# Kernel tuning notes

Measured on AMD Instinct MI355X. Metric: run time of the kernel, lower is better.

## Reference

```python
import jax, jax.numpy as jnp
import numpy as np
import math

EPS = 1e-6


def setup_inputs() -> dict:
    key = jax.random.key(0)
    k1, k2, k3 = jax.random.split(key, 3)
    B, S, D = 8, 2048, 256
    return {
        "query": jax.random.normal(k1, (B, S, D), dtype=jnp.float32),
        "keys": jax.random.normal(k2, (B, S, D), dtype=jnp.float32),
        "values": jax.random.normal(k3, (B, S, D), dtype=jnp.float32),
        "c": jnp.asarray(0.01, dtype=jnp.float32),  # learned curvature parameter
    }


def reference(query, keys, values, c):
    # query/keys: [B,S,D], values: [B,S,Dv]
    scale = math.sqrt(query.shape[-1])
    q2 = jnp.sum(query * query, axis=-1)            # [B,S]  |q_i|^2
    k2 = jnp.sum(keys * keys, axis=-1)              # [B,S]  |k_j|^2
    cross = jnp.einsum("bid,bjd->bij", query, keys)  # [B,S,S]
    # squared pairwise distance via identity, avoiding the [B,S,S,D] diff tensor
    nd2 = jnp.maximum(q2[:, :, None] + k2[:, None, :] - 2.0 * cross, 0.0)
    # faithful to original: denom pairs query row i with key row i (broadcast quirk)
    denom = jnp.maximum((1.0 - c * q2) * (1.0 - c * k2), EPS)  # [B,S]
    arg = jnp.maximum(1.0 + 2.0 * c * nd2 / denom[:, :, None], 1.0 + EPS)
    dist = jnp.arccosh(arg)                          # [B,S,S]
    attn = jax.nn.softmax(-dist / scale, axis=-1)
    return jnp.einsum("bij,bjd->bid", attn, values)
```

## Files before the change

kernel.cpp:

```cpp
#include <hip/hip_runtime.h>

#define B_N   8
#define S_LEN 2048
#define D_DIM 256

typedef __attribute__((ext_vector_type(4)))  float          f32x4;
typedef __attribute__((ext_vector_type(16))) float          f32x16;
typedef __attribute__((ext_vector_type(8)))  short          s16x8;
typedef __attribute__((ext_vector_type(8)))  __bf16         b16x8;
typedef __attribute__((ext_vector_type(8)))  unsigned short u16x8;
typedef __attribute__((ext_vector_type(4)))  unsigned int   u32x4;

__device__ __forceinline__ unsigned short f2bf(float f) {
    unsigned u = __builtin_bit_cast(unsigned, f);
    u += 0x7FFFu + ((u >> 16) & 1u);
    return (unsigned short)(u >> 16);
}
__device__ __forceinline__ u16x8 pack8(f32x4 a, f32x4 b) {
    u16x8 o;
#pragma unroll
    for (int u = 0; u < 4; ++u) { o[u] = f2bf(a[u]); o[u + 4] = f2bf(b[u]); }
    return o;
}
__device__ __forceinline__ f32x16 zero16() {
    f32x16 z;
#pragma unroll
    for (int i = 0; i < 16; ++i) z[i] = 0.f;
    return z;
}
__device__ __forceinline__ unsigned cvtpk(float lo, float hi) {
    unsigned r;
    asm("v_cvt_pk_bf16_f32 %0, %1, %2" : "=v"(r) : "v"(lo), "v"(hi));
    return r;
}
__device__ __forceinline__ void xswap(unsigned& x, unsigned& y, int lh) {
    unsigned vs = lh ? x : y;
    unsigned vr = (unsigned)__shfl_xor((int)vs, 32, 64);
    x = lh ? vr : x;
    y = lh ? y : vr;
}
__device__ __forceinline__ float hw_sqrt(float x) {
    float r; asm("v_sqrt_f32 %0, %1" : "=v"(r) : "v"(x)); return r;
}
__device__ __forceinline__ float hw_log2(float x) {
    float r; asm("v_log_f32 %0, %1" : "=v"(r) : "v"(x)); return r;
}
__device__ __forceinline__ float hw_exp2(float x) {
    float r; asm("v_exp_f32 %0, %1" : "=v"(r) : "v"(x)); return r;
}
__device__ __forceinline__ float hw_rcp(float x) {
    float r; asm("v_rcp_f32 %0, %1" : "=v"(r) : "v"(x)); return r;
}
__device__ __forceinline__ void gload16(const void* g, void* l) {
    __builtin_amdgcn_global_load_lds((const __attribute__((address_space(1))) void*)g,
                                     (__attribute__((address_space(3))) void*)l, 16, 0, 0);
}

template <typename A>
__device__ __forceinline__ auto mfma3216_(A a, A b, f32x16 c, int)
    -> decltype(__builtin_amdgcn_mfma_f32_32x32x16_bf16(a, b, c, 0, 0, 0)) {
    return __builtin_amdgcn_mfma_f32_32x32x16_bf16(a, b, c, 0, 0, 0);
}
template <typename A>
__device__ __forceinline__ f32x16 mfma3216_(A a, A b, f32x16 c, long) {
    b16x8 a2 = __builtin_bit_cast(b16x8, a);
    b16x8 b2 = __builtin_bit_cast(b16x8, b);
    return __builtin_amdgcn_mfma_f32_32x32x16_bf16(a2, b2, c, 0, 0, 0);
}
__device__ __forceinline__ f32x16 MFMA(u16x8 a, u16x8 b, f32x16 c) {
    return mfma3216_(__builtin_bit_cast(s16x8, a), __builtin_bit_cast(s16x8, b), c, 0);
}

__global__ void __launch_bounds__(256) prep_rows(const float* __restrict__ Q,
                                                 const float* __restrict__ K,
                                                 const float* __restrict__ cp,
                                                 float* __restrict__ q2g,
                                                 float* __restrict__ k2g,
                                                 float* __restrict__ cfg) {
    const int w = threadIdx.x >> 6, l = threadIdx.x & 63;
    const float c = *cp;
#pragma unroll 1
    for (int p = 0; p < 16; ++p) {
        const int row = blockIdx.x * 64 + p * 4 + w;
        f32x4 qv = *((const f32x4*)(Q + (size_t)row * D_DIM) + l);
        f32x4 kv = *((const f32x4*)(K + (size_t)row * D_DIM) + l);
        float sq = qv[0]*qv[0] + qv[1]*qv[1] + qv[2]*qv[2] + qv[3]*qv[3];
        float sk = kv[0]*kv[0] + kv[1]*kv[1] + kv[2]*kv[2] + kv[3]*kv[3];
#pragma unroll
        for (int m = 1; m < 64; m <<= 1) {
            sq += __shfl_xor(sq, m, 64);
            sk += __shfl_xor(sk, m, 64);
        }
        if (l == 0) {
            q2g[row] = sq;
            k2g[row] = sk;
            float dn = fmaxf((1.f - c * sq) * (1.f - c * sk), 1e-6f);
            cfg[row] = 2.f * c / dn;
        }
    }
}

__global__ void __launch_bounds__(256) cvt_bf16(const float* __restrict__ src,
                                                unsigned short* __restrict__ dst) {
    const size_t i = ((size_t)blockIdx.x * 256 + threadIdx.x) * 8;
    f32x4 a = *(const f32x4*)(src + i);
    f32x4 b = *(const f32x4*)(src + i + 4);
    *(u16x8*)(dst + i) = pack8(a, b);
}

__global__ void __launch_bounds__(256) transp_v(const float* __restrict__ V,
                                                unsigned short* __restrict__ VT) {
    __shared__ float tile[64][65];
    const int bid = blockIdx.x;
    const int b = bid >> 7, rem = bid & 127, jt = rem >> 2, dt = rem & 3;
    const int j0 = jt * 64, d0 = dt * 64;
    const int t = threadIdx.x;
#pragma unroll
    for (int p = 0; p < 4; ++p) {
        const int jr = p * 16 + (t >> 4);
        f32x4 v = *(const f32x4*)(V + (size_t)(b * S_LEN + j0 + jr) * D_DIM + d0 + (t & 15) * 4);
#pragma unroll
        for (int u = 0; u < 4; ++u) tile[jr][(t & 15) * 4 + u] = v[u];
    }
    __syncthreads();
#pragma unroll
    for (int p = 0; p < 2; ++p) {
        const int dr = p * 32 + (t >> 3), seg = t & 7;
        u16x8 o;
#pragma unroll
        for (int u = 0; u < 8; ++u) o[u] = f2bf(tile[seg * 8 + u][dr]);
        *(u16x8*)(VT + (size_t)(b * D_DIM + d0 + dr) * S_LEN + j0 + seg * 8) = o;
    }
}

template <int PRE>
__global__ void __launch_bounds__(256, 2) hyp_attn(
    const float* __restrict__ Qf, const float* __restrict__ Kf, const float* __restrict__ Vf,
    const unsigned short* __restrict__ Kb, const unsigned short* __restrict__ VTg,
    const float* __restrict__ q2g, const float* __restrict__ k2g, const float* __restrict__ cfg,
    float* __restrict__ out) {
    __shared__ __align__(1024) unsigned char tiles[65536];
    __shared__ float k2sh[S_LEN];
    __shared__ float lsumBuf[2][2][32];
    const int bid = blockIdx.x;
    const int nb = (bid & 7) * 64 + (bid >> 3);
    const int b = nb >> 6, rt = nb & 63;
    const int tid = threadIdx.x;
    const int w = tid >> 6, l = tid & 63;
    const int l31 = l & 31, lh = l >> 5;
    const int jsub = w & 1, dh = w >> 1;
    const int qr0 = rt * 32;
    const int qrow = b * S_LEN + qr0 + l31;

    *(f32x4*)&k2sh[tid * 8]     = *(const f32x4*)(k2g + b * S_LEN + tid * 8);
    *(f32x4*)&k2sh[tid * 8 + 4] = *(const f32x4*)(k2g + b * S_LEN + tid * 8 + 4);

    u16x8 qf[16];
    {
        const float* qp = Qf + (size_t)qrow * D_DIM + lh * 8;
#pragma unroll
        for (int ks = 0; ks < 16; ++ks) {
            f32x4 a = *(const f32x4*)(qp + ks * 16);
            f32x4 c4 = *(const f32x4*)(qp + ks * 16 + 4);
            qf[ks] = pack8(a, c4);
        }
    }
    const float q2r = q2g[qrow];
    const float cfr = cfg[qrow];
    const float base1 = fmaf(cfr, q2r, 1.0f);

    f32x16 oacc[4];
#pragma unroll
    for (int i = 0; i < 4; ++i) oacc[i] = zero16();
    float lsum = 0.f;

    const size_t kbBase = (size_t)b * S_LEN * D_DIM;

    auto stageK = [&](int buf, int it) {
        const int j0 = it * 64;
#pragma unroll
        for (int p = 0; p < 8; ++p) {
            const int idx = p * 256 + tid;
            const int row = idx >> 5, sl = idx & 31;
            const unsigned short* gp = Kb + kbBase + (size_t)(j0 + row) * D_DIM
                                     + ((sl ^ (row & 7)) << 3);
            gload16(gp, (char*)tiles + buf * 32768 + idx * 16);
        }
    };
    auto stageK0 = [&](int buf, int it) {
        const int j0 = it * 64;
#pragma unroll
        for (int p = 0; p < 8; ++p) {
            const int idx = p * 256 + tid;
            const int row = idx >> 5, sl = idx & 31;
            const float* sp = Kf + kbBase + (size_t)(j0 + row) * D_DIM
                            + ((sl ^ (row & 7)) << 3);
            *(u16x8*)((char*)tiles + buf * 32768 + idx * 16) =
                pack8(*(const f32x4*)sp, *(const f32x4*)(sp + 4));
        }
    };
    const unsigned short* vbase = VTg + ((size_t)(b * D_DIM + dh * 128 + l31) * S_LEN)
                                + jsub * 32 + lh * 8;
    auto loadVg = [&](int it, u16x8 (&Vr)[8]) {
        const unsigned short* p0 = vbase + it * 64;
#pragma unroll
        for (int db = 0; db < 4; ++db) {
            Vr[db * 2]     = *(const u16x8*)(p0 + (size_t)(db * 32) * S_LEN);
            Vr[db * 2 + 1] = *(const u16x8*)(p0 + (size_t)(db * 32) * S_LEN + 16);
        }
    };
    auto loadV0 = [&](int it, u16x8 (&Vr)[8]) {
        const int j0 = it * 64 + jsub * 32 + lh * 8;
#pragma unroll
        for (int db = 0; db < 4; ++db) {
            const int d = dh * 128 + db * 32 + l31;
            u16x8 o0, o1;
#pragma unroll
            for (int u = 0; u < 8; ++u) {
                o0[u] = f2bf(Vf[kbBase + (size_t)(j0 + u) * D_DIM + d]);
                o1[u] = f2bf(Vf[kbBase + (size_t)(j0 + 16 + u) * D_DIM + d]);
            }
            Vr[db * 2] = o0; Vr[db * 2 + 1] = o1;
        }
    };

    const int xk = (l31 & 7) << 4;
    const char* KBp = (const char*)tiles + (jsub * 32 + l31) * 512;

    auto qktF = [&](int buf) {
        f32x16 s = zero16();
#pragma unroll
        for (int ks = 0; ks < 16; ++ks) {
            u16x8 kf = *(const u16x8*)(KBp + buf * 32768 + (((ks * 2 + lh) << 4) ^ xk));
            s = MFMA(kf, qf[ks], s);
        }
        return s;
    };
    auto softmaxF = [&](int it, f32x16& s, u16x8& pa0, u16x8& pa1) {
        f32x4 k2q[4];
#pragma unroll
        for (int g = 0; g < 4; ++g)
            k2q[g] = *(const f32x4*)&k2sh[it * 64 + jsub * 32 + g * 8 + lh * 4];
#pragma unroll
        for (int r = 0; r < 16; ++r) {
            const float t = fmaf(-2.f, s[r], k2q[r >> 2][r & 3]);
            const float arg = fmaxf(fmaf(cfr, t, base1), 1.f + 1e-6f);
            const float y = arg + hw_sqrt(fmaf(arg, arg, -1.f));
            const float p = hw_exp2(hw_log2(y) * -0.0625f);
            lsum += p;
            s[r] = p;
        }
        unsigned A_ = cvtpk(s[0], s[1]),   C_ = cvtpk(s[2], s[3]);
        unsigned Bv = cvtpk(s[4], s[5]),   D_ = cvtpk(s[6], s[7]);
        unsigned E_ = cvtpk(s[8], s[9]),   G_ = cvtpk(s[10], s[11]);
        unsigned F_ = cvtpk(s[12], s[13]), H_ = cvtpk(s[14], s[15]);
        xswap(A_, Bv, lh); xswap(C_, D_, lh);
        xswap(E_, F_, lh); xswap(G_, H_, lh);
        pa0 = __builtin_bit_cast(u16x8, (u32x4){A_, C_, Bv, D_});
        pa1 = __builtin_bit_cast(u16x8, (u32x4){E_, G_, F_, H_});
    };
    auto pvF = [&](u16x8 pa0, u16x8 pa1, u16x8 (&VA)[8]) {
#pragma unroll
        for (int db = 0; db < 4; ++db) {
            oacc[db] = MFMA(pa0, VA[db * 2], oacc[db]);
            oacc[db] = MFMA(pa1, VA[db * 2 + 1], oacc[db]);
        }
    };

    if (PRE) {
        stageK(0, 0);
        asm volatile("s_waitcnt vmcnt(0) lgkmcnt(0)" ::: "memory");
        __builtin_amdgcn_s_barrier();
        f32x16 sacc = qktF(0);
#pragma unroll 1
        for (int it = 0; it < 32; ++it) {
            u16x8 VA[8];
            loadVg(it, VA);
            if (it < 31) stageK((it + 1) & 1, it + 1);
            u16x8 pa0, pa1;
            softmaxF(it, sacc, pa0, pa1);
            asm volatile("s_waitcnt vmcnt(0)" ::: "memory");
            __builtin_amdgcn_s_barrier();
            __builtin_amdgcn_s_setprio(1);
            pvF(pa0, pa1, VA);
            if (it < 31) sacc = qktF((it + 1) & 1);
            __builtin_amdgcn_s_setprio(0);
        }
    } else {
#pragma unroll 1
        for (int it = 0; it < 32; ++it) {
            u16x8 VA[8];
            stageK0(0, it);
            loadV0(it, VA);
            __syncthreads();
            f32x16 sacc = qktF(0);
            u16x8 pa0, pa1;
            softmaxF(it, sacc, pa0, pa1);
            pvF(pa0, pa1, VA);
            __syncthreads();
        }
    }

    lsum += __shfl_xor(lsum, 32, 64);
    if (lh == 0) lsumBuf[jsub][dh][l31] = lsum;
    float* sf = (float*)tiles;
    if (jsub == 1) {
#pragma unroll
        for (int db = 0; db < 4; ++db)
#pragma unroll
            for (int r = 0; r < 16; ++r) {
                const int crow = (r & 3) + 8 * (r >> 2) + 4 * lh;
                sf[dh * 4096 + crow * 128 + db * 32 + l31] = oacc[db][r];
            }
    }
    __syncthreads();
    if (jsub == 0) {
        float rdn[16];
#pragma unroll
        for (int r = 0; r < 16; ++r) {
            const int crow = (r & 3) + 8 * (r >> 2) + 4 * lh;
            rdn[r] = hw_rcp(lsumBuf[0][dh][crow] + lsumBuf[1][dh][crow]);
        }
#pragma unroll
        for (int db = 0; db < 4; ++db)
#pragma unroll
            for (int r = 0; r < 16; ++r) {
                const int crow = (r & 3) + 8 * (r >> 2) + 4 * lh;
                const float o = oacc[db][r] + sf[dh * 4096 + crow * 128 + db * 32 + l31];
                out[(size_t)(b * S_LEN + qr0 + crow) * D_DIM + dh * 128 + db * 32 + l31]
                    = o * rdn[r];
            }
    }
}

extern "C" void kernel_launch(void* const* d_in, const int* in_sizes, int n_in,
                              void* d_out, int out_size, void* d_ws, size_t ws_size,
                              hipStream_t stream) {
    const float* Q = (const float*)d_in[0];
    const float* K = (const float*)d_in[1];
    const float* V = (const float*)d_in[2];
    const float* cp = (const float*)d_in[3];
    float* out = (float*)d_out;
    (void)in_sizes; (void)n_in; (void)out_size;

    const size_t BS = (size_t)B_N * S_LEN;
    float* q2g = (float*)d_ws;
    float* k2g = q2g + BS;
    float* cfg = k2g + BS;
    unsigned short* Kb = (unsigned short*)(cfg + BS);
    unsigned short* VTg = Kb + BS * D_DIM;
    const size_t need_full = 3 * BS * 4 + 2 * BS * D_DIM * 2;

    prep_rows<<<(B_N * S_LEN) / 64, 256, 0, stream>>>(Q, K, cp, q2g, k2g, cfg);

    if (ws_size >= need_full) {
        cvt_bf16<<<(int)((BS * D_DIM / 8) / 256), 256, 0, stream>>>(K, Kb);
        transp_v<<<B_N * (S_LEN / 64) * (D_DIM / 64), 256, 0, stream>>>(V, VTg);
        hyp_attn<1><<<512, 256, 0, stream>>>(Q, K, V, Kb, VTg, q2g, k2g, cfg, out);
    } else {
        hyp_attn<0><<<512, 256, 0, stream>>>(Q, K, V, Kb, VTg, q2g, k2g, cfg, out);
    }
}
```

Baseline: 122.4 us.

## Share 128-key K tiles across 64 query rows per 512-thread block

```diff
diff --git a/kernel.cpp b/kernel.cpp
--- a/kernel.cpp
+++ b/kernel.cpp
@@ -134,26 +134,25 @@
 }
 
 template <int PRE>
-__global__ void __launch_bounds__(256, 2) hyp_attn(
+__global__ void __launch_bounds__(512, 2) hyp_attn(
     const float* __restrict__ Qf, const float* __restrict__ Kf, const float* __restrict__ Vf,
     const unsigned short* __restrict__ Kb, const unsigned short* __restrict__ VTg,
     const float* __restrict__ q2g, const float* __restrict__ k2g, const float* __restrict__ cfg,
     float* __restrict__ out) {
-    __shared__ __align__(1024) unsigned char tiles[65536];
+    __shared__ __align__(1024) unsigned char tiles[131072];
     __shared__ float k2sh[S_LEN];
     __shared__ float lsumBuf[2][2][32];
     const int bid = blockIdx.x;
-    const int nb = (bid & 7) * 64 + (bid >> 3);
-    const int b = nb >> 6, rt = nb & 63;
+    const int nb = (bid & 7) * 32 + (bid >> 3);
+    const int b = nb >> 5, rt = nb & 31;
     const int tid = threadIdx.x;
     const int w = tid >> 6, l = tid & 63;
     const int l31 = l & 31, lh = l >> 5;
-    const int jsub = w & 1, dh = w >> 1;
-    const int qr0 = rt * 32;
+    const int qg = w >> 2, jsub = (w >> 1) & 1, dh = w & 1;
+    const int qr0 = rt * 64 + qg * 32;
     const int qrow = b * S_LEN + qr0 + l31;
 
-    *(f32x4*)&k2sh[tid * 8]     = *(const f32x4*)(k2g + b * S_LEN + tid * 8);
-    *(f32x4*)&k2sh[tid * 8 + 4] = *(const f32x4*)(k2g + b * S_LEN + tid * 8 + 4);
+    *(f32x4*)&k2sh[tid * 4] = *(const f32x4*)(k2g + b * S_LEN + tid * 4);
 
     u16x8 qf[16];
     {
@@ -177,40 +176,40 @@
     const size_t kbBase = (size_t)b * S_LEN * D_DIM;
 
     auto stageK = [&](int buf, int it) {
-        const int j0 = it * 64;
+        const int j0 = it * 128;
 #pragma unroll
         for (int p = 0; p < 8; ++p) {
-            const int idx = p * 256 + tid;
+            const int idx = p * 512 + tid;
             const int row = idx >> 5, sl = idx & 31;
             const unsigned short* gp = Kb + kbBase + (size_t)(j0 + row) * D_DIM
                                      + ((sl ^ (row & 7)) << 3);
-            gload16(gp, (char*)tiles + buf * 32768 + idx * 16);
-        }
-    };
-    auto stageK0 = [&](int buf, int it) {
-        const int j0 = it * 64;
+            gload16(gp, (char*)tiles + buf * 65536 + idx * 16);
+        }
+    };
+    auto stageK0 = [&](int it) {
+        const int j0 = it * 128;
 #pragma unroll
         for (int p = 0; p < 8; ++p) {
-            const int idx = p * 256 + tid;
+            const int idx = p * 512 + tid;
             const int row = idx >> 5, sl = idx & 31;
             const float* sp = Kf + kbBase + (size_t)(j0 + row) * D_DIM
                             + ((sl ^ (row & 7)) << 3);
-            *(u16x8*)((char*)tiles + buf * 32768 + idx * 16) =
+            *(u16x8*)((char*)tiles + idx * 16) =
                 pack8(*(const f32x4*)sp, *(const f32x4*)(sp + 4));
         }
     };
     const unsigned short* vbase = VTg + ((size_t)(b * D_DIM + dh * 128 + l31) * S_LEN)
                                 + jsub * 32 + lh * 8;
-    auto loadVg = [&](int it, u16x8 (&Vr)[8]) {
-        const unsigned short* p0 = vbase + it * 64;
+    auto loadVg = [&](int it, int half, u16x8 (&Vr)[8]) {
+        const unsigned short* p0 = vbase + it * 128 + half * 64;
 #pragma unroll
         for (int db = 0; db < 4; ++db) {
             Vr[db * 2]     = *(const u16x8*)(p0 + (size_t)(db * 32) * S_LEN);
             Vr[db * 2 + 1] = *(const u16x8*)(p0 + (size_t)(db * 32) * S_LEN + 16);
         }
     };
-    auto loadV0 = [&](int it, u16x8 (&Vr)[8]) {
-        const int j0 = it * 64 + jsub * 32 + lh * 8;
+    auto loadV0 = [&](int it, int half, u16x8 (&Vr)[8]) {
+        const int j0 = it * 128 + half * 64 + jsub * 32 + lh * 8;
 #pragma unroll
         for (int db = 0; db < 4; ++db) {
             const int d = dh * 128 + db * 32 + l31;
@@ -225,22 +224,23 @@
     };
 
     const int xk = (l31 & 7) << 4;
-    const char* KBp = (const char*)tiles + (jsub * 32 + l31) * 512;
-
-    auto qktF = [&](int buf) {
+
+    auto qktF = [&](int buf, int half) {
+        const char* base = (const char*)tiles + buf * 65536
+                         + (half * 64 + jsub * 32 + l31) * 512;
         f32x16 s = zero16();
 #pragma unroll
         for (int ks = 0; ks < 16; ++ks) {
-            u16x8 kf = *(const u16x8*)(KBp + buf * 32768 + (((ks * 2 + lh) << 4) ^ xk));
+            u16x8 kf = *(const u16x8*)(base + (((ks * 2 + lh) << 4) ^ xk));
             s = MFMA(kf, qf[ks], s);
         }
         return s;
     };
-    auto softmaxF = [&](int it, f32x16& s, u16x8& pa0, u16x8& pa1) {
+    auto softmaxF = [&](int it, int half, f32x16& s, u16x8& pa0, u16x8& pa1) {
         f32x4 k2q[4];
 #pragma unroll
         for (int g = 0; g < 4; ++g)
-            k2q[g] = *(const f32x4*)&k2sh[it * 64 + jsub * 32 + g * 8 + lh * 4];
+            k2q[g] = *(const f32x4*)&k2sh[it * 128 + half * 64 + jsub * 32 + g * 8 + lh * 4];
 #pragma unroll
         for (int r = 0; r < 16; ++r) {
             const float t = fmaf(-2.f, s[r], k2q[r >> 2][r & 3]);
@@ -271,46 +271,59 @@
         stageK(0, 0);
         asm volatile("s_waitcnt vmcnt(0) lgkmcnt(0)" ::: "memory");
         __builtin_amdgcn_s_barrier();
-        f32x16 sacc = qktF(0);
 #pragma unroll 1
-        for (int it = 0; it < 32; ++it) {
-            u16x8 VA[8];
-            loadVg(it, VA);
-            if (it < 31) stageK((it + 1) & 1, it + 1);
+        for (int it = 0; it < 16; ++it) {
+            const int buf = it & 1;
+            u16x8 VA[8], VB[8];
+            loadVg(it, 0, VA);
+            loadVg(it, 1, VB);
+            if (it < 15) stageK(buf ^ 1, it + 1);
+            f32x16 sacc = qktF(buf, 0);
             u16x8 pa0, pa1;
-            softmaxF(it, sacc, pa0, pa1);
+            softmaxF(it, 0, sacc, pa0, pa1);
+            __builtin_amdgcn_s_setprio(1);
+            pvF(pa0, pa1, VA);
+            __builtin_amdgcn_s_setprio(0);
+            f32x16 sbcc = qktF(buf, 1);
+            u16x8 pb0, pb1;
+            softmaxF(it, 1, sbcc, pb0, pb1);
+            __builtin_amdgcn_s_setprio(1);
+            pvF(pb0, pb1, VB);
+            __builtin_amdgcn_s_setprio(0);
             asm volatile("s_waitcnt vmcnt(0)" ::: "memory");
             __builtin_amdgcn_s_barrier();
-            __builtin_amdgcn_s_setprio(1);
-            pvF(pa0, pa1, VA);
-            if (it < 31) sacc = qktF((it + 1) & 1);
-            __builtin_amdgcn_s_setprio(0);
         }
     } else {
 #pragma unroll 1
-        for (int it = 0; it < 32; ++it) {
-            u16x8 VA[8];
-            stageK0(0, it);
-            loadV0(it, VA);
+        for (int it = 0; it < 16; ++it) {
+            u16x8 VA[8], VB[8];
+            stageK0(it);
+            loadV0(it, 0, VA);
+            loadV0(it, 1, VB);
             __syncthreads();
-            f32x16 sacc = qktF(0);
+            f32x16 sacc = qktF(0, 0);
             u16x8 pa0, pa1;
-            softmaxF(it, sacc, pa0, pa1);
+            softmaxF(it, 0, sacc, pa0, pa1);
             pvF(pa0, pa1, VA);
+            f32x16 sbcc = qktF(0, 1);
+            u16x8 pb0, pb1;
+            softmaxF(it, 1, sbcc, pb0, pb1);
+            pvF(pb0, pb1, VB);
             __syncthreads();
         }
     }
 
     lsum += __shfl_xor(lsum, 32, 64);
-    if (lh == 0) lsumBuf[jsub][dh][l31] = lsum;
+    if (lh == 0 && dh == 0) lsumBuf[jsub][qg][l31] = lsum;
     float* sf = (float*)tiles;
+    __syncthreads();
     if (jsub == 1) {
 #pragma unroll
         for (int db = 0; db < 4; ++db)
 #pragma unroll
             for (int r = 0; r < 16; ++r) {
                 const int crow = (r & 3) + 8 * (r >> 2) + 4 * lh;
-                sf[dh * 4096 + crow * 128 + db * 32 + l31] = oacc[db][r];
+                sf[(qg * 2 + dh) * 4096 + crow * 128 + db * 32 + l31] = oacc[db][r];
             }
     }
     __syncthreads();
@@ -319,14 +332,15 @@
 #pragma unroll
         for (int r = 0; r < 16; ++r) {
             const int crow = (r & 3) + 8 * (r >> 2) + 4 * lh;
-            rdn[r] = hw_rcp(lsumBuf[0][dh][crow] + lsumBuf[1][dh][crow]);
+            rdn[r] = hw_rcp(lsumBuf[0][qg][crow] + lsumBuf[1][qg][crow]);
         }
 #pragma unroll
         for (int db = 0; db < 4; ++db)
 #pragma unroll
             for (int r = 0; r < 16; ++r) {
                 const int crow = (r & 3) + 8 * (r >> 2) + 4 * lh;
-                const float o = oacc[db][r] + sf[dh * 4096 + crow * 128 + db * 32 + l31];
+                const float o = oacc[db][r]
+                              + sf[(qg * 2 + dh) * 4096 + crow * 128 + db * 32 + l31];
                 out[(size_t)(b * S_LEN + qr0 + crow) * D_DIM + dh * 128 + db * 32 + l31]
                     = o * rdn[r];
             }
@@ -356,8 +370,8 @@
     if (ws_size >= need_full) {
         cvt_bf16<<<(int)((BS * D_DIM / 8) / 256), 256, 0, stream>>>(K, Kb);
         transp_v<<<B_N * (S_LEN / 64) * (D_DIM / 64), 256, 0, stream>>>(V, VTg);
-        hyp_attn<1><<<512, 256, 0, stream>>>(Q, K, V, Kb, VTg, q2g, k2g, cfg, out);
+        hyp_attn<1><<<256, 512, 0, stream>>>(Q, K, V, Kb, VTg, q2g, k2g, cfg, out);
     } else {
-        hyp_attn<0><<<512, 256, 0, stream>>>(Q, K, V, Kb, VTg, q2g, k2g, cfg, out);
-    }
-}
+        hyp_attn<0><<<256, 512, 0, stream>>>(Q, K, V, Kb, VTg, q2g, k2g, cfg, out);
+    }
+}
```

Measured after the change: 199.7 us. +63.1%, slower.
